# Kernel tuning notes

Measured on AMD Instinct MI355X. Metric: run time of the kernel, lower is better.

## Reference

```python
import jax, jax.numpy as jnp
import numpy as np

K = 20  # hard-coded in LPDNet


def act(v):
    # LeakyReLU with negative_slope=0.0 == ReLU
    return jnp.maximum(v, 0.0)


def conv1d(x, w, b):
    # x: (B,C,N), w: (O,C), b: (O,) -> (B,O,N)  (1x1 Conv1d)
    return jnp.einsum('bcn,oc->bon', x, w) + b[None, :, None]


def conv2d(x, w, b):
    # x: (B,C,N,K), w: (O,C), b: (O,) -> (B,O,N,K)  (1x1 Conv2d)
    return jnp.einsum('bcnk,oc->bonk', x, w) + b[None, :, None, None]


def knn(x, k):
    # x: (B,C,N) -> idx (B,N,k) of nearest neighbors by negative squared L2
    xx = jnp.sum(x * x, axis=1)                       # (B,N)
    inner = jnp.einsum('bcn,bcm->bnm', x, x)          # (B,N,N)
    pairwise = 2.0 * inner - xx[:, :, None] - xx[:, None, :]
    _, idx = jax.lax.top_k(pairwise, k)
    return idx


def graph_feature(x, idx):
    # x: (B,C,N), idx: (B,N,k) -> (B,2C,N,k) as concat(neighbor - center, center)
    xt = jnp.transpose(x, (0, 2, 1))                  # (B,N,C)
    nbr = jax.vmap(lambda f, i: f[i])(xt, idx)        # (B,N,k,C)
    ctr = jnp.broadcast_to(xt[:, :, None, :], nbr.shape)
    feat = jnp.concatenate([nbr - ctr, ctr], axis=-1)  # (B,N,k,2C)
    return jnp.transpose(feat, (0, 3, 1, 2))          # (B,2C,N,k)


def setup_inputs():
    key = jax.random.key(0)
    ks = jax.random.split(key, 13)
    p = lambda k, s: jax.random.normal(k, s, jnp.float32) * 0.02
    return {
        'x': jax.random.normal(ks[0], (8, 1, 4096, 3), jnp.float32),
        'w1': p(ks[1], (64, 3)),    'b1': p(ks[2], (64,)),
        'w2': p(ks[3], (64, 64)),   'b2': p(ks[4], (64,)),
        'wdg1': p(ks[5], (128, 128)), 'bdg1': p(ks[6], (128,)),
        'wdg2': p(ks[7], (128, 128)), 'bdg2': p(ks[8], (128,)),
        'wsn1': p(ks[9], (256, 256)), 'bsn1': p(ks[10], (256,)),
        'w3': p(ks[11], (1024, 512)), 'b3': p(ks[12], (1024,)),
    }


def reference(x, w1, b1, w2, b2, wdg1, bdg1, wdg2, bdg2, wsn1, bsn1, w3, b3):
    xp = jnp.transpose(jnp.squeeze(x, 1), (0, 2, 1))  # (B,3,N)
    xinit = xp
    h = act(conv1d(xp, w1, b1))                       # (B,64,N)
    h = act(conv1d(h, w2, b2))                        # (B,64,N)
    idx1 = knn(h, K)
    g = graph_feature(h, idx1)                        # (B,128,N,K)
    g = act(conv2d(g, wdg1, bdg1))                    # (B,128,N,K)
    x1 = jnp.max(g, axis=-1)                          # (B,128,N)
    g = act(conv2d(g, wdg2, bdg2))                    # (B,128,N,K)
    x2 = jnp.max(g, axis=-1)                          # (B,128,N)
    idx2 = knn(xinit, K)                              # knn on raw 3D coords
    g = graph_feature(x2, idx2)                       # (B,256,N,K)
    g = act(conv2d(g, wsn1, bsn1))                    # (B,256,N,K)
    x3 = jnp.max(g, axis=-1)                          # (B,256,N)
    cat = jnp.concatenate([x1, x2, x3], axis=1)       # (B,512,N)
    out = act(conv1d(cat, w3, b3))                    # (B,1024,N)
    return out[..., None]                             # (B,1024,N,1)
```

## Files before the change

### kernel.cpp

```cpp
#include <hip/hip_runtime.h>
#include <stdint.h>


#define NB 8
#define NP 4096
#define NPTS (NB*NP)

typedef float  floatx4 __attribute__((ext_vector_type(4)));
typedef short  short8  __attribute__((ext_vector_type(8)));

__device__ __forceinline__ unsigned short f2bf(float f) {
  union { float f; uint32_t u; } v; v.f = f;
  uint32_t r = v.u + 0x7fffu + ((v.u >> 16) & 1u);
  return (unsigned short)(r >> 16);
}
__device__ __forceinline__ float bf2f(unsigned short h) {
  union { uint32_t u; float f; } v; v.u = ((uint32_t)h) << 16;
  return v.f;
}

__device__ __forceinline__ floatx4 mfma_bf16(short8 a, short8 b, floatx4 c) {
  return __builtin_amdgcn_mfma_f32_16x16x32_bf16(a, b, c, 0, 0, 0);
}

__global__ void cvt_weights(const float* wdg1, unsigned short* wdg1b,
                            const float* wdg2, unsigned short* wdg2b,
                            const float* wsn1, unsigned short* wsn1b,
                            const float* w3, unsigned short* w3b) {
  int i = blockIdx.x * 256 + threadIdx.x;
  if (i < 16384) {
    int c = i & 127;
    wdg1b[i] = f2bf(wdg1[i] - (c >= 64 ? wdg1[i - 64] : 0.f));
  }
  if (i < 16384) wdg2b[i] = f2bf(wdg2[i]);
  if (i < 65536) {
    int c = i & 255;
    wsn1b[i] = f2bf(wsn1[i] - (c >= 128 ? wsn1[i - 128] : 0.f));
  }
  if (i < 524288) w3b[i] = f2bf(w3[i]);
}

__global__ __launch_bounds__(256) void conv12(
    const float* __restrict__ xin, const float* __restrict__ w1,
    const float* __restrict__ b1, const float* __restrict__ w2,
    const float* __restrict__ b2,
    unsigned short* __restrict__ hb16, unsigned short* __restrict__ hlo16,
    float* __restrict__ hh, float* __restrict__ cc) {
  int wave = threadIdx.x >> 6, lane = threadIdx.x & 63;
  int p = blockIdx.x * 4 + wave;
  __shared__ float s_h1[4][64];
  const float* xp = xin + p * 3;
  float c0 = xp[0], c1 = xp[1], c2 = xp[2];
  float v = b1[lane] + w1[lane*3+0]*c0 + w1[lane*3+1]*c1 + w1[lane*3+2]*c2;
  s_h1[wave][lane] = fmaxf(v, 0.f);
  __syncthreads();
  float acc = b2[lane];
  const float* wr = w2 + lane * 64;
  #pragma unroll
  for (int c = 0; c < 64; c += 4) {
    floatx4 w4 = *(const floatx4*)(wr + c);
    acc += w4[0]*s_h1[wave][c]   + w4[1]*s_h1[wave][c+1]
         + w4[2]*s_h1[wave][c+2] + w4[3]*s_h1[wave][c+3];
  }
  acc = fmaxf(acc, 0.f);
  unsigned short hi = f2bf(acc);
  hb16[p*64 + lane] = hi;
  hlo16[p*64 + lane] = f2bf(acc - bf2f(hi));
  float sq = acc * acc;
  #pragma unroll
  for (int off = 32; off; off >>= 1) sq += __shfl_xor(sq, off, 64);
  if (lane == 0) { hh[p] = sq; cc[p] = c0*c0 + c1*c1 + c2*c2; }
}

__global__ __launch_bounds__(256) void knn64_mfma(
    const unsigned short* __restrict__ Hhi, const unsigned short* __restrict__ Hlo,
    const float* __restrict__ XX, int* __restrict__ idx_out) {
  __shared__ unsigned short mhi[64][72];
  __shared__ unsigned short mlo[64][72];
  __shared__ float dots[64][68];
  __shared__ float xxR[64];
  __shared__ float xxM[64];
  __shared__ float tau[64];
  int b = blockIdx.y;
  int r0 = blockIdx.x * 64;
  int t = threadIdx.x;
  int lane = t & 63, wave = t >> 6;
  int quad = lane >> 4, l15 = lane & 15;
  const unsigned short* Hhib = Hhi + (size_t)b * NP * 64;
  const unsigned short* Hlob = Hlo + (size_t)b * NP * 64;
  short8 ahi[2], alo[2];
  {
    const unsigned short* pr = Hhib + (size_t)(r0 + wave * 16 + l15) * 64 + quad * 8;
    const unsigned short* pl = Hlob + (size_t)(r0 + wave * 16 + l15) * 64 + quad * 8;
    ahi[0] = *(const short8*)pr; ahi[1] = *(const short8*)(pr + 32);
    alo[0] = *(const short8*)pl; alo[1] = *(const short8*)(pl + 32);
  }
  if (t < 64) { xxR[t] = XX[b * NP + r0 + t]; tau[t] = -__builtin_inff(); }

  float lv[20]; int li[20];
  #pragma unroll
  for (int s = 0; s < 20; s++) { lv[s] = -__builtin_inff(); li[s] = 0x7fffffff; }
  float minval = -__builtin_inff(); int minpos = 0;
  int row = t >> 2, sub = t & 3;

  for (int mt = 0; mt < NP / 64; mt++) {
    int m0 = mt * 64;
    {
      int pt = t >> 2, c0 = (t & 3) * 16;
      const unsigned short* sh = Hhib + (size_t)(m0 + pt) * 64 + c0;
      const unsigned short* sl = Hlob + (size_t)(m0 + pt) * 64 + c0;
      *(short8*)&mhi[pt][c0]     = *(const short8*)sh;
      *(short8*)&mhi[pt][c0 + 8] = *(const short8*)(sh + 8);
      *(short8*)&mlo[pt][c0]     = *(const short8*)sl;
      *(short8*)&mlo[pt][c0 + 8] = *(const short8*)(sl + 8);
    }
    if (t < 64) xxM[t] = XX[b * NP + m0 + t];
    __syncthreads();
    #pragma unroll
    for (int nt = 0; nt < 4; nt++) {
      floatx4 acc = (floatx4)0.f;
      #pragma unroll
      for (int ks = 0; ks < 2; ks++) {
        int k0 = ks * 32 + quad * 8;
        short8 bhi = *(short8*)&mhi[nt * 16 + l15][k0];
        short8 blo = *(short8*)&mlo[nt * 16 + l15][k0];
        acc = mfma_bf16(ahi[ks], bhi, acc);
        acc = mfma_bf16(ahi[ks], blo, acc);
        acc = mfma_bf16(alo[ks], bhi, acc);
        acc = mfma_bf16(alo[ks], blo, acc);
      }
      int colg = nt * 16 + l15;
      float xm = xxM[colg];
      #pragma unroll
      for (int r = 0; r < 4; r++) {
        int mr = wave * 16 + quad * 4 + r;
        dots[mr][colg] = 2.f * acc[r] - xxR[mr] - xm;
      }
    }
    __syncthreads();
    float gate = fmaxf(minval, tau[row]);
    floatx4 dv0 = *(floatx4*)&dots[row][sub * 16];
    floatx4 dv1 = *(floatx4*)&dots[row][sub * 16 + 4];
    floatx4 dv2 = *(floatx4*)&dots[row][sub * 16 + 8];
    floatx4 dv3 = *(floatx4*)&dots[row][sub * 16 + 12];
    uint32_t mask = 0;
    #pragma unroll
    for (int j = 0; j < 4; j++) {
      if (dv0[j] > gate) mask |= 1u << j;
      if (dv1[j] > gate) mask |= 1u << (4 + j);
      if (dv2[j] > gate) mask |= 1u << (8 + j);
      if (dv3[j] > gate) mask |= 1u << (12 + j);
    }
    #pragma clang loop unroll(disable)
    for (int round = 0; round < 16; round++) {
      if (!__any(mask != 0)) break;
      if (mask) {
        int i = __builtin_ctz(mask); mask &= mask - 1;
        float v = dots[row][sub * 16 + i];
        if (v > minval) {
          int gi = m0 + sub * 16 + i;
          #pragma unroll
          for (int s = 0; s < 20; s++)
            if (s == minpos) { lv[s] = v; li[s] = gi; }
          minval = __builtin_inff();
          #pragma unroll
          for (int s = 0; s < 20; s++)
            if (lv[s] < minval) { minval = lv[s]; minpos = s; }
        }
      }
    }
    tau[row] = fmaxf(tau[row], minval);
  }
  int base = (b * NP + r0 + row) * 20;
  for (int sel = 0; sel < 20; sel++) {
    float mybv = -__builtin_inff(); int mybi = 0x7fffffff, mybs = 0;
    #pragma unroll
    for (int s = 0; s < 20; s++) {
      bool better = lv[s] > mybv || (lv[s] == mybv && li[s] < mybi);
      if (better) { mybv = lv[s]; mybi = li[s]; mybs = s; }
    }
    float bv = mybv; int bi = mybi;
    float ov = __shfl_xor(bv, 1, 64); int oi = __shfl_xor(bi, 1, 64);
    if (ov > bv || (ov == bv && oi < bi)) { bv = ov; bi = oi; }
    ov = __shfl_xor(bv, 2, 64); oi = __shfl_xor(bi, 2, 64);
    if (ov > bv || (ov == bv && oi < bi)) { bv = ov; bi = oi; }
    if (sub == 0) idx_out[base + sel] = bi;
    if (bi == mybi) {
      #pragma unroll
      for (int s = 0; s < 20; s++)
        if (s == mybs) { lv[s] = -__builtin_inff(); li[s] = 0x7fffffff; }
    }
  }
}

template<int C>
__global__ __launch_bounds__(256) void knn_topk(
    const float* __restrict__ X, const float* __restrict__ XX,
    int* __restrict__ idx_out) {
  __shared__ float rowsT[C][68];
  __shared__ float mT[C][68];
  __shared__ float dots[64][68];
  __shared__ float xxR[64];
  __shared__ float xxM[64];
  __shared__ float tau[64];
  int b = blockIdx.y;
  int r0 = blockIdx.x * 64;
  int t = threadIdx.x;
  const float* Xb = X + (size_t)b * NP * C;
  for (int e = t; e < C * 64; e += 256) {
    int r = e / C, c = e - r * C;
    rowsT[c][r] = Xb[(r0 + r) * C + c];
  }
  if (t < 64) { xxR[t] = XX[b * NP + r0 + t]; tau[t] = -__builtin_inff(); }

  float lv[20]; int li[20];
  #pragma unroll
  for (int s = 0; s < 20; s++) { lv[s] = -__builtin_inff(); li[s] = 0x7fffffff; }
  float minval = -__builtin_inff(); int minpos = 0;

  int tm = t & 15, tr = t >> 4;
  int row = t >> 2, sub = t & 3;

  for (int mt = 0; mt < NP / 64; mt++) {
    int m0 = mt * 64;
    for (int e = t; e < C * 64; e += 256) {
      int r = e / C, c = e - r * C;
      mT[c][r] = Xb[(m0 + r) * C + c];
    }
    if (t < 64) xxM[t] = XX[b * NP + m0 + t];
    __syncthreads();
    float acc[4][4];
    #pragma unroll
    for (int i = 0; i < 4; i++)
      #pragma unroll
      for (int j = 0; j < 4; j++) acc[i][j] = 0.f;
    for (int c = 0; c < C; c++) {
      floatx4 av = *(floatx4*)&rowsT[c][tr * 4];
      floatx4 bv = *(floatx4*)&mT[c][tm * 4];
      #pragma unroll
      for (int i = 0; i < 4; i++)
        #pragma unroll
        for (int j = 0; j < 4; j++) acc[i][j] += av[i] * bv[j];
    }
    #pragma unroll
    for (int i = 0; i < 4; i++) {
      floatx4 sv;
      #pragma unroll
      for (int j = 0; j < 4; j++)
        sv[j] = 2.f * acc[i][j] - xxR[tr*4 + i] - xxM[tm*4 + j];
      *(floatx4*)&dots[tr*4 + i][tm*4] = sv;
    }
    __syncthreads();
    float gate = fmaxf(minval, tau[row]);
    floatx4 dv0 = *(floatx4*)&dots[row][sub * 16];
    floatx4 dv1 = *(floatx4*)&dots[row][sub * 16 + 4];
    floatx4 dv2 = *(floatx4*)&dots[row][sub * 16 + 8];
    floatx4 dv3 = *(floatx4*)&dots[row][sub * 16 + 12];
    uint32_t mask = 0;
    #pragma unroll
    for (int j = 0; j < 4; j++) {
      if (dv0[j] > gate) mask |= 1u << j;
      if (dv1[j] > gate) mask |= 1u << (4 + j);
      if (dv2[j] > gate) mask |= 1u << (8 + j);
      if (dv3[j] > gate) mask |= 1u << (12 + j);
    }
    #pragma clang loop unroll(disable)
    for (int round = 0; round < 16; round++) {
      if (!__any(mask != 0)) break;
      if (mask) {
        int i = __builtin_ctz(mask); mask &= mask - 1;
        float v = dots[row][sub * 16 + i];
        if (v > minval) {
          int gi = m0 + sub * 16 + i;
          #pragma unroll
          for (int s = 0; s < 20; s++)
            if (s == minpos) { lv[s] = v; li[s] = gi; }
          minval = __builtin_inff();
          #pragma unroll
          for (int s = 0; s < 20; s++)
            if (lv[s] < minval) { minval = lv[s]; minpos = s; }
        }
      }
    }
    tau[row] = fmaxf(tau[row], minval);
  }
  int base = (b * NP + r0 + row) * 20;
  for (int sel = 0; sel < 20; sel++) {
    float mybv = -__builtin_inff(); int mybi = 0x7fffffff, mybs = 0;
    #pragma unroll
    for (int s = 0; s < 20; s++) {
      bool better = lv[s] > mybv || (lv[s] == mybv && li[s] < mybi);
      if (better) { mybv = lv[s]; mybi = li[s]; mybs = s; }
    }
    float bv = mybv; int bi = mybi;
    float ov = __shfl_xor(bv, 1, 64); int oi = __shfl_xor(bi, 1, 64);
    if (ov > bv || (ov == bv && oi < bi)) { bv = ov; bi = oi; }
    ov = __shfl_xor(bv, 2, 64); oi = __shfl_xor(bi, 2, 64);
    if (ov > bv || (ov == bv && oi < bi)) { bv = ov; bi = oi; }
    if (sub == 0) idx_out[base + sel] = bi;
    if (bi == mybi) {
      #pragma unroll
      for (int s = 0; s < 20; s++)
        if (s == mybs) { lv[s] = -__builtin_inff(); li[s] = 0x7fffffff; }
    }
  }
}

__global__ __launch_bounds__(256) void dg_stage(
    const unsigned short* __restrict__ hb16, const int* __restrict__ idx1,
    const unsigned short* __restrict__ w1b, const float* __restrict__ bia1,
    const unsigned short* __restrict__ w2b, const float* __restrict__ bia2,
    unsigned short* __restrict__ featb) {
  __shared__ unsigned short s_a[80][136];
  __shared__ unsigned short s_v[80][136];
  __shared__ int s_nbf[80];
  int p0 = blockIdx.x * 4;
  int b = p0 >> 12, n0 = p0 & 4095;
  int t = threadIdx.x;
  int lane = t & 63, wave = t >> 6;
  if (t < 80) s_nbf[t] = idx1[p0 * 20 + t];
  __syncthreads();
  const unsigned short* hbb = hb16 + (size_t)b * NP * 64;
  {
    int cc = (t & 15) * 8;
    int r00 = t >> 4;
    #pragma unroll
    for (int it = 0; it < 5; it++) {
      int row = r00 + it * 16;
      const unsigned short* src = (cc < 64)
        ? hbb + (size_t)s_nbf[row] * 64 + cc
        : hbb + (size_t)(n0 + row / 20) * 64 + (cc - 64);
      *(short8*)&s_a[row][cc] = *(const short8*)src;
    }
  }
  __syncthreads();
  int quad = lane >> 4, mrow = lane & 15;
  int nblock = wave * 32;
  {
    floatx4 acc[5][2];
    #pragma unroll
    for (int mt = 0; mt < 5; mt++) { acc[mt][0] = (floatx4)0.f; acc[mt][1] = (floatx4)0.f; }
    #pragma unroll
    for (int ks = 0; ks < 4; ks++) {
      int k0 = ks * 32 + quad * 8;
      short8 w0 = *(const short8*)(w1b + (nblock + mrow) * 128 + k0);
      short8 w1v = *(const short8*)(w1b + (nblock + 16 + mrow) * 128 + k0);
      #pragma unroll
      for (int mt = 0; mt < 5; mt++) {
        short8 a = *(short8*)&s_a[mt * 16 + mrow][k0];
        acc[mt][0] = mfma_bf16(a, w0, acc[mt][0]);
        acc[mt][1] = mfma_bf16(a, w1v, acc[mt][1]);
      }
    }
    #pragma unroll
    for (int ns = 0; ns < 2; ns++) {
      int o = nblock + ns * 16 + mrow;
      float bz = bia1[o];
      #pragma unroll
      for (int mt = 0; mt < 5; mt++)
        #pragma unroll
        for (int r = 0; r < 4; r++)
          s_v[mt * 16 + quad * 4 + r][o] = f2bf(fmaxf(acc[mt][ns][r] + bz, 0.f));
    }
  }
  __syncthreads();
  #pragma unroll
  for (int it = 0; it < 2; it++) {
    int e = t + it * 256;
    int pt = e >> 7, o = e & 127;
    float mx = 0.f;
    for (int k = 0; k < 20; k++) mx = fmaxf(mx, bf2f(s_v[pt * 20 + k][o]));
    featb[(size_t)(p0 + pt) * 512 + o] = f2bf(mx);
  }
  {
    floatx4 acc[5][2];
    #pragma unroll
    for (int mt = 0; mt < 5; mt++) { acc[mt][0] = (floatx4)0.f; acc[mt][1] = (floatx4)0.f; }
    #pragma unroll
    for (int ks = 0; ks < 4; ks++) {
      int k0 = ks * 32 + quad * 8;
      short8 w0 = *(const short8*)(w2b + (nblock + mrow) * 128 + k0);
      short8 w1v = *(const short8*)(w2b + (nblock + 16 + mrow) * 128 + k0);
      #pragma unroll
      for (int mt = 0; mt < 5; mt++) {
        short8 a = *(short8*)&s_v[mt * 16 + mrow][k0];
        acc[mt][0] = mfma_bf16(a, w0, acc[mt][0]);
        acc[mt][1] = mfma_bf16(a, w1v, acc[mt][1]);
      }
    }
    #pragma unroll
    for (int ns = 0; ns < 2; ns++) {
      int o = nblock + ns * 16 + mrow;
      float bz = bia2[o];
      #pragma unroll
      for (int mt = 0; mt < 5; mt++)
        #pragma unroll
        for (int r = 0; r < 4; r++)
          s_a[mt * 16 + quad * 4 + r][o] = f2bf(fmaxf(acc[mt][ns][r] + bz, 0.f));
    }
  }
  __syncthreads();
  #pragma unroll
  for (int it = 0; it < 2; it++) {
    int e = t + it * 256;
    int pt = e >> 7, o = e & 127;
    float mx = 0.f;
    for (int k = 0; k < 20; k++) mx = fmaxf(mx, bf2f(s_a[pt * 20 + k][o]));
    featb[(size_t)(p0 + pt) * 512 + 128 + o] = f2bf(mx);
  }
}

__global__ __launch_bounds__(256) void sn_stage(
    const int* __restrict__ idx2, const unsigned short* __restrict__ wb,
    const float* __restrict__ bias, unsigned short* __restrict__ featb) {
  __shared__ unsigned short s_a[80][264];
  __shared__ int s_nbf[80];
  int p0 = blockIdx.x * 4;
  int b = p0 >> 12, n0 = p0 & 4095;
  int bb = b << 12;
  int t = threadIdx.x;
  int lane = t & 63, wave = t >> 6;
  if (t < 80) s_nbf[t] = idx2[p0 * 20 + t];
  __syncthreads();
  {
    int cc = (t & 31) * 8;
    int r00 = t >> 5;
    #pragma unroll
    for (int it = 0; it < 10; it++) {
      int row = r00 + it * 8;
      const unsigned short* src = (cc < 128)
        ? featb + (size_t)(bb + s_nbf[row]) * 512 + 128 + cc
        : featb + (size_t)(bb + n0 + row / 20) * 512 + cc;
      *(short8*)&s_a[row][cc] = *(const short8*)src;
    }
  }
  __syncthreads();
  int quad = lane >> 4, mrow = lane & 15;
  int nblock = wave * 64;
  floatx4 acc[5][4];
  #pragma unroll
  for (int mt = 0; mt < 5; mt++)
    #pragma unroll
    for (int ns = 0; ns < 4; ns++) acc[mt][ns] = (floatx4)0.f;
  #pragma unroll
  for (int ks = 0; ks < 8; ks++) {
    int k0 = ks * 32 + quad * 8;
    short8 w[4];
    #pragma unroll
    for (int ns = 0; ns < 4; ns++)
      w[ns] = *(const short8*)(wb + (nblock + ns * 16 + mrow) * 256 + k0);
    #pragma unroll
    for (int mt = 0; mt < 5; mt++) {
      short8 a = *(short8*)&s_a[mt * 16 + mrow][k0];
      #pragma unroll
      for (int ns = 0; ns < 4; ns++)
        acc[mt][ns] = mfma_bf16(a, w[ns], acc[mt][ns]);
    }
  }
  __syncthreads();
  #pragma unroll
  for (int ns = 0; ns < 4; ns++) {
    int o = nblock + ns * 16 + mrow;
    float bz = bias[o];
    #pragma unroll
    for (int mt = 0; mt < 5; mt++)
      #pragma unroll
      for (int r = 0; r < 4; r++)
        s_a[mt * 16 + quad * 4 + r][o] = f2bf(fmaxf(acc[mt][ns][r] + bz, 0.f));
  }
  __syncthreads();
  #pragma unroll
  for (int it = 0; it < 4; it++) {
    int e = t + it * 256;
    int pt = e >> 8, o = e & 255;
    float mx = 0.f;
    for (int k = 0; k < 20; k++) mx = fmaxf(mx, bf2f(s_a[pt * 20 + k][o]));
    featb[(size_t)(p0 + pt) * 512 + 256 + o] = f2bf(mx);
  }
}

__global__ __launch_bounds__(256) void conv3_gemm(
    const unsigned short* __restrict__ w3b, const unsigned short* __restrict__ featb,
    const float* __restrict__ b3, float* __restrict__ out) {
  __shared__ unsigned short s_a[128][40];
  __shared__ unsigned short s_b[128][40];
  int o0 = blockIdx.x * 128, p0 = blockIdx.y * 128;
  int t = threadIdx.x, lane = t & 63, wave = t >> 6;
  int wy = wave >> 1, wx = wave & 1;
  int quad = lane >> 4, l15 = lane & 15;
  floatx4 acc[4][4];
  #pragma unroll
  for (int i = 0; i < 4; i++)
    #pragma unroll
    for (int j = 0; j < 4; j++) acc[i][j] = (floatx4)0.f;
  for (int kc = 0; kc < 16; kc++) {
    __syncthreads();
    for (int e = t; e < 512; e += 256) {
      int r = e >> 2, c8 = (e & 3) * 8;
      *(short8*)&s_a[r][c8] = *(const short8*)(w3b + (size_t)(o0 + r) * 512 + kc * 32 + c8);
    }
    for (int e = t; e < 512; e += 256) {
      int r = e >> 2, c8 = (e & 3) * 8;
      *(short8*)&s_b[r][c8] = *(const short8*)(featb + (size_t)(p0 + r) * 512 + kc * 32 + c8);
    }
    __syncthreads();
    int k0 = quad * 8;
    short8 af[4], bfr[4];
    #pragma unroll
    for (int i = 0; i < 4; i++) af[i] = *(short8*)&s_a[wy * 64 + i * 16 + l15][k0];
    #pragma unroll
    for (int j = 0; j < 4; j++) bfr[j] = *(short8*)&s_b[wx * 64 + j * 16 + l15][k0];
    #pragma unroll
    for (int i = 0; i < 4; i++)
      #pragma unroll
      for (int j = 0; j < 4; j++) acc[i][j] = mfma_bf16(af[i], bfr[j], acc[i][j]);
  }
  #pragma unroll
  for (int i = 0; i < 4; i++)
    #pragma unroll
    for (int j = 0; j < 4; j++) {
      int pl = p0 + wx * 64 + j * 16 + l15;
      int bI = pl >> 12, n = pl & 4095;
      #pragma unroll
      for (int r = 0; r < 4; r++) {
        int o = o0 + wy * 64 + i * 16 + quad * 4 + r;
        out[(size_t)(bI * 1024 + o) * 4096 + n] = fmaxf(acc[i][j][r] + b3[o], 0.f);
      }
    }
}

extern "C" void kernel_launch(void* const* d_in, const int* in_sizes, int n_in,
                              void* d_out, int out_size, void* d_ws, size_t ws_size,
                              hipStream_t stream) {
  const float* x    = (const float*)d_in[0];
  const float* w1   = (const float*)d_in[1];
  const float* b1   = (const float*)d_in[2];
  const float* w2   = (const float*)d_in[3];
  const float* b2   = (const float*)d_in[4];
  const float* wdg1 = (const float*)d_in[5];
  const float* bdg1 = (const float*)d_in[6];
  const float* wdg2 = (const float*)d_in[7];
  const float* bdg2 = (const float*)d_in[8];
  const float* wsn1 = (const float*)d_in[9];
  const float* bsn1 = (const float*)d_in[10];
  const float* w3   = (const float*)d_in[11];
  const float* b3   = (const float*)d_in[12];

  float* ws = (float*)d_ws;
  unsigned short* hlo16 = (unsigned short*)ws;
  float* hh = ws + 2097152;
  float* cc = ws + 2129920;
  int* idx1 = (int*)(ws + 2162688);
  int* idx2 = (int*)(ws + 2818048);
  unsigned short* featb = (unsigned short*)(ws + 3473408);
  unsigned short* wdg1b = (unsigned short*)(ws + 11862016);
  unsigned short* wdg2b = (unsigned short*)(ws + 11870208);
  unsigned short* wsn1b = (unsigned short*)(ws + 11878400);
  unsigned short* w3b   = (unsigned short*)(ws + 11911168);
  unsigned short* hb16  = (unsigned short*)(ws + 12173312);

  cvt_weights<<<2048, 256, 0, stream>>>(wdg1, wdg1b, wdg2, wdg2b,
                                        wsn1, wsn1b, w3, w3b);
  conv12<<<8192, 256, 0, stream>>>(x, w1, b1, w2, b2, hb16, hlo16, hh, cc);
  knn64_mfma<<<dim3(64, 8), 256, 0, stream>>>(hb16, hlo16, hh, idx1);
  knn_topk<3><<<dim3(64, 8), 256, 0, stream>>>(x, cc, idx2);
  dg_stage<<<8192, 256, 0, stream>>>(hb16, idx1, wdg1b, bdg1, wdg2b, bdg2, featb);
  sn_stage<<<8192, 256, 0, stream>>>(idx2, wsn1b, bsn1, featb);
  conv3_gemm<<<dim3(8, 256), 256, 0, stream>>>(w3b, featb, b3, (float*)d_out);
}
```

Measured before the change: 1.077 ms.

## Split KNN candidate scan into two halves and merge partial top-20 lists

Both KNN kernels now run on a grid with a z dimension of 2, each block scanning half of the candidate points and writing a sorted partial top-20 (values and indices) to workspace. A new merge40 kernel merges the two sorted lists per row into the final 20 indices. This doubles the block count from 512 to 1024 so the GPU's compute units are better occupied, at the cost of extra global writes, two extra launches, and reusing the featb workspace region as temporary storage.

```diff
diff --git a/kernel.cpp b/kernel.cpp
--- a/kernel.cpp
+++ b/kernel.cpp
@@ -74,7 +74,8 @@
 
 __global__ __launch_bounds__(256) void knn64_mfma(
     const unsigned short* __restrict__ Hhi, const unsigned short* __restrict__ Hlo,
-    const float* __restrict__ XX, int* __restrict__ idx_out) {
+    const float* __restrict__ XX, float* __restrict__ val_out,
+    int* __restrict__ idxp_out) {
   __shared__ unsigned short mhi[64][72];
   __shared__ unsigned short mlo[64][72];
   __shared__ float dots[64][68];
@@ -83,6 +84,7 @@
   __shared__ float tau[64];
   int b = blockIdx.y;
   int r0 = blockIdx.x * 64;
+  int half = blockIdx.z;
   int t = threadIdx.x;
   int lane = t & 63, wave = t >> 6;
   int quad = lane >> 4, l15 = lane & 15;
@@ -103,7 +105,8 @@
   float minval = -__builtin_inff(); int minpos = 0;
   int row = t >> 2, sub = t & 3;
 
-  for (int mt = 0; mt < NP / 64; mt++) {
+  int mt0 = half * (NP / 128);
+  for (int mt = mt0; mt < mt0 + NP / 128; mt++) {
     int m0 = mt * 64;
     {
       int pt = t >> 2, c0 = (t & 3) * 16;
@@ -171,7 +174,7 @@
     }
     tau[row] = fmaxf(tau[row], minval);
   }
-  int base = (b * NP + r0 + row) * 20;
+  int base = ((b * NP + r0 + row) * 2 + half) * 20;
   for (int sel = 0; sel < 20; sel++) {
     float mybv = -__builtin_inff(); int mybi = 0x7fffffff, mybs = 0;
     #pragma unroll
@@ -184,7 +187,7 @@
     if (ov > bv || (ov == bv && oi < bi)) { bv = ov; bi = oi; }
     ov = __shfl_xor(bv, 2, 64); oi = __shfl_xor(bi, 2, 64);
     if (ov > bv || (ov == bv && oi < bi)) { bv = ov; bi = oi; }
-    if (sub == 0) idx_out[base + sel] = bi;
+    if (sub == 0) { val_out[base + sel] = bv; idxp_out[base + sel] = bi; }
     if (bi == mybi) {
       #pragma unroll
       for (int s = 0; s < 20; s++)
@@ -196,7 +199,7 @@
 template<int C>
 __global__ __launch_bounds__(256) void knn_topk(
     const float* __restrict__ X, const float* __restrict__ XX,
-    int* __restrict__ idx_out) {
+    float* __restrict__ val_out, int* __restrict__ idxp_out) {
   __shared__ float rowsT[C][68];
   __shared__ float mT[C][68];
   __shared__ float dots[64][68];
@@ -205,6 +208,7 @@
   __shared__ float tau[64];
   int b = blockIdx.y;
   int r0 = blockIdx.x * 64;
+  int half = blockIdx.z;
   int t = threadIdx.x;
   const float* Xb = X + (size_t)b * NP * C;
   for (int e = t; e < C * 64; e += 256) {
@@ -221,7 +225,8 @@
   int tm = t & 15, tr = t >> 4;
   int row = t >> 2, sub = t & 3;
 
-  for (int mt = 0; mt < NP / 64; mt++) {
+  int mt0 = half * (NP / 128);
+  for (int mt = mt0; mt < mt0 + NP / 128; mt++) {
     int m0 = mt * 64;
     for (int e = t; e < C * 64; e += 256) {
       int r = e / C, c = e - r * C;
@@ -284,7 +289,7 @@
     }
     tau[row] = fmaxf(tau[row], minval);
   }
-  int base = (b * NP + r0 + row) * 20;
+  int base = ((b * NP + r0 + row) * 2 + half) * 20;
   for (int sel = 0; sel < 20; sel++) {
     float mybv = -__builtin_inff(); int mybi = 0x7fffffff, mybs = 0;
     #pragma unroll
@@ -297,12 +302,30 @@
     if (ov > bv || (ov == bv && oi < bi)) { bv = ov; bi = oi; }
     ov = __shfl_xor(bv, 2, 64); oi = __shfl_xor(bi, 2, 64);
     if (ov > bv || (ov == bv && oi < bi)) { bv = ov; bi = oi; }
-    if (sub == 0) idx_out[base + sel] = bi;
+    if (sub == 0) { val_out[base + sel] = bv; idxp_out[base + sel] = bi; }
     if (bi == mybi) {
       #pragma unroll
       for (int s = 0; s < 20; s++)
         if (s == mybs) { lv[s] = -__builtin_inff(); li[s] = 0x7fffffff; }
     }
+  }
+}
+
+__global__ __launch_bounds__(256) void merge40(
+    const float* __restrict__ val, const int* __restrict__ midx,
+    int* __restrict__ idx_out) {
+  int r = blockIdx.x * 256 + threadIdx.x;
+  const float* vA = val + (size_t)r * 40;
+  const int*   iA = midx + (size_t)r * 40;
+  int a = 0, bp = 20;
+  int base = r * 20;
+  #pragma unroll
+  for (int s = 0; s < 20; s++) {
+    float va = vA[a], vb = vA[bp];
+    int ia = iA[a], ib = iA[bp];
+    bool takeA = (va > vb) || (va == vb && ia < ib);
+    idx_out[base + s] = takeA ? ia : ib;
+    if (takeA) a++; else bp++;
   }
 }
 
@@ -559,11 +582,18 @@
   unsigned short* w3b   = (unsigned short*)(ws + 11911168);
   unsigned short* hb16  = (unsigned short*)(ws + 12173312);
 
+  float* c1val = ws + 3473408;
+  int*   c1idx = (int*)(ws + 4784128);
+  float* c2val = ws + 6094848;
+  int*   c2idx = (int*)(ws + 7405568);
+
   cvt_weights<<<2048, 256, 0, stream>>>(wdg1, wdg1b, wdg2, wdg2b,
                                         wsn1, wsn1b, w3, w3b);
   conv12<<<8192, 256, 0, stream>>>(x, w1, b1, w2, b2, hb16, hlo16, hh, cc);
-  knn64_mfma<<<dim3(64, 8), 256, 0, stream>>>(hb16, hlo16, hh, idx1);
-  knn_topk<3><<<dim3(64, 8), 256, 0, stream>>>(x, cc, idx2);
+  knn64_mfma<<<dim3(64, 8, 2), 256, 0, stream>>>(hb16, hlo16, hh, c1val, c1idx);
+  knn_topk<3><<<dim3(64, 8, 2), 256, 0, stream>>>(x, cc, c2val, c2idx);
+  merge40<<<128, 256, 0, stream>>>(c1val, c1idx, idx1);
+  merge40<<<128, 256, 0, stream>>>(c2val, c2idx, idx2);
   dg_stage<<<8192, 256, 0, stream>>>(hb16, idx1, wdg1b, bdg1, wdg2b, bdg2, featb);
   sn_stage<<<8192, 256, 0, stream>>>(idx2, wsn1b, bsn1, featb);
   conv3_gemm<<<dim3(8, 256), 256, 0, stream>>>(w3b, featb, b3, (float*)d_out);
```

Measured after the change: 1.101 ms. 2.2% more time.

## Widen kNN column tile to 128 and drop row-constant distance terms

Applied to the files above, without the earlier changes.

The MFMA kNN kernel now processes 128 candidate columns per iteration instead of 64, halving the number of loop iterations and barriers and giving each lane 32 candidates to scan. Both kNN kernels replace the score 2*dot - xx_r - xx_m with dot - 0.5*xx_m. The dropped term is constant per row and the rest is a positive rescale, so the ranking is unchanged. The wider tile increases shared memory and register use (8 float4 per thread), which may reduce occupancy, and the rescaled score can change tie behaviour slightly due to rounding.

```diff
diff --git a/kernel.cpp b/kernel.cpp
--- a/kernel.cpp
+++ b/kernel.cpp
@@ -75,11 +75,10 @@
 __global__ __launch_bounds__(256) void knn64_mfma(
     const unsigned short* __restrict__ Hhi, const unsigned short* __restrict__ Hlo,
     const float* __restrict__ XX, int* __restrict__ idx_out) {
-  __shared__ unsigned short mhi[64][72];
-  __shared__ unsigned short mlo[64][72];
-  __shared__ float dots[64][68];
-  __shared__ float xxR[64];
-  __shared__ float xxM[64];
+  __shared__ unsigned short mhi[128][72];
+  __shared__ unsigned short mlo[128][72];
+  __shared__ float dots[64][132];
+  __shared__ float xxMh[128];
   __shared__ float tau[64];
   int b = blockIdx.y;
   int r0 = blockIdx.x * 64;
@@ -95,7 +94,7 @@
     ahi[0] = *(const short8*)pr; ahi[1] = *(const short8*)(pr + 32);
     alo[0] = *(const short8*)pl; alo[1] = *(const short8*)(pl + 32);
   }
-  if (t < 64) { xxR[t] = XX[b * NP + r0 + t]; tau[t] = -__builtin_inff(); }
+  if (t < 64) tau[t] = -__builtin_inff();
 
   float lv[20]; int li[20];
   #pragma unroll
@@ -103,21 +102,26 @@
   float minval = -__builtin_inff(); int minpos = 0;
   int row = t >> 2, sub = t & 3;
 
-  for (int mt = 0; mt < NP / 64; mt++) {
-    int m0 = mt * 64;
+  for (int mt = 0; mt < NP / 128; mt++) {
+    int m0 = mt * 128;
     {
-      int pt = t >> 2, c0 = (t & 3) * 16;
-      const unsigned short* sh = Hhib + (size_t)(m0 + pt) * 64 + c0;
-      const unsigned short* sl = Hlob + (size_t)(m0 + pt) * 64 + c0;
-      *(short8*)&mhi[pt][c0]     = *(const short8*)sh;
-      *(short8*)&mhi[pt][c0 + 8] = *(const short8*)(sh + 8);
-      *(short8*)&mlo[pt][c0]     = *(const short8*)sl;
-      *(short8*)&mlo[pt][c0 + 8] = *(const short8*)(sl + 8);
-    }
-    if (t < 64) xxM[t] = XX[b * NP + m0 + t];
+      int hf = t & 1, r = (t >> 1) & 127;
+      int c0 = hf * 32;
+      const unsigned short* sh = Hhib + (size_t)(m0 + r) * 64 + c0;
+      const unsigned short* sl = Hlob + (size_t)(m0 + r) * 64 + c0;
+      *(short8*)&mhi[r][c0]      = *(const short8*)sh;
+      *(short8*)&mhi[r][c0 + 8]  = *(const short8*)(sh + 8);
+      *(short8*)&mhi[r][c0 + 16] = *(const short8*)(sh + 16);
+      *(short8*)&mhi[r][c0 + 24] = *(const short8*)(sh + 24);
+      *(short8*)&mlo[r][c0]      = *(const short8*)sl;
+      *(short8*)&mlo[r][c0 + 8]  = *(const short8*)(sl + 8);
+      *(short8*)&mlo[r][c0 + 16] = *(const short8*)(sl + 16);
+      *(short8*)&mlo[r][c0 + 24] = *(const short8*)(sl + 24);
+    }
+    if (t < 128) xxMh[t] = 0.5f * XX[b * NP + m0 + t];
     __syncthreads();
     #pragma unroll
-    for (int nt = 0; nt < 4; nt++) {
+    for (int nt = 0; nt < 8; nt++) {
       floatx4 acc = (floatx4)0.f;
       #pragma unroll
       for (int ks = 0; ks < 2; ks++) {
@@ -130,12 +134,121 @@
         acc = mfma_bf16(alo[ks], blo, acc);
       }
       int colg = nt * 16 + l15;
-      float xm = xxM[colg];
+      float xm = xxMh[colg];
       #pragma unroll
       for (int r = 0; r < 4; r++) {
         int mr = wave * 16 + quad * 4 + r;
-        dots[mr][colg] = 2.f * acc[r] - xxR[mr] - xm;
-      }
+        dots[mr][colg] = acc[r] - xm;
+      }
+    }
+    __syncthreads();
+    float gate = fmaxf(minval, tau[row]);
+    floatx4 dv[8];
+    #pragma unroll
+    for (int q = 0; q < 8; q++) dv[q] = *(floatx4*)&dots[row][sub * 32 + q * 4];
+    uint32_t mask = 0;
+    #pragma unroll
+    for (int q = 0; q < 8; q++)
+      #pragma unroll
+      for (int j = 0; j < 4; j++)
+        if (dv[q][j] > gate) mask |= 1u << (q * 4 + j);
+    #pragma clang loop unroll(disable)
+    for (int round = 0; round < 32; round++) {
+      if (!__any(mask != 0)) break;
+      if (mask) {
+        int i = __builtin_ctz(mask); mask &= mask - 1;
+        float v = dots[row][sub * 32 + i];
+        if (v > minval) {
+          int gi = m0 + sub * 32 + i;
+          #pragma unroll
+          for (int s = 0; s < 20; s++)
+            if (s == minpos) { lv[s] = v; li[s] = gi; }
+          minval = __builtin_inff();
+          #pragma unroll
+          for (int s = 0; s < 20; s++)
+            if (lv[s] < minval) { minval = lv[s]; minpos = s; }
+        }
+      }
+    }
+    tau[row] = fmaxf(tau[row], minval);
+  }
+  int base = (b * NP + r0 + row) * 20;
+  for (int sel = 0; sel < 20; sel++) {
+    float mybv = -__builtin_inff(); int mybi = 0x7fffffff, mybs = 0;
+    #pragma unroll
+    for (int s = 0; s < 20; s++) {
+      bool better = lv[s] > mybv || (lv[s] == mybv && li[s] < mybi);
+      if (better) { mybv = lv[s]; mybi = li[s]; mybs = s; }
+    }
+    float bv = mybv; int bi = mybi;
+    float ov = __shfl_xor(bv, 1, 64); int oi = __shfl_xor(bi, 1, 64);
+    if (ov > bv || (ov == bv && oi < bi)) { bv = ov; bi = oi; }
+    ov = __shfl_xor(bv, 2, 64); oi = __shfl_xor(bi, 2, 64);
+    if (ov > bv || (ov == bv && oi < bi)) { bv = ov; bi = oi; }
+    if (sub == 0) idx_out[base + sel] = bi;
+    if (bi == mybi) {
+      #pragma unroll
+      for (int s = 0; s < 20; s++)
+        if (s == mybs) { lv[s] = -__builtin_inff(); li[s] = 0x7fffffff; }
+    }
+  }
+}
+
+template<int C>
+__global__ __launch_bounds__(256) void knn_topk(
+    const float* __restrict__ X, const float* __restrict__ XX,
+    int* __restrict__ idx_out) {
+  __shared__ float rowsT[C][68];
+  __shared__ float mT[C][68];
+  __shared__ float dots[64][68];
+  __shared__ float xxMh[64];
+  __shared__ float tau[64];
+  int b = blockIdx.y;
+  int r0 = blockIdx.x * 64;
+  int t = threadIdx.x;
+  const float* Xb = X + (size_t)b * NP * C;
+  for (int e = t; e < C * 64; e += 256) {
+    int r = e / C, c = e - r * C;
+    rowsT[c][r] = Xb[(r0 + r) * C + c];
+  }
+  if (t < 64) tau[t] = -__builtin_inff();
+
+  float lv[20]; int li[20];
+  #pragma unroll
+  for (int s = 0; s < 20; s++) { lv[s] = -__builtin_inff(); li[s] = 0x7fffffff; }
+  float minval = -__builtin_inff(); int minpos = 0;
+
+  int tm = t & 15, tr = t >> 4;
+  int row = t >> 2, sub = t & 3;
+
+  for (int mt = 0; mt < NP / 64; mt++) {
+    int m0 = mt * 64;
+    for (int e = t; e < C * 64; e += 256) {
+      int r = e / C, c = e - r * C;
+      mT[c][r] = Xb[(m0 + r) * C + c];
+    }
+    if (t < 64) xxMh[t] = 0.5f * XX[b * NP + m0 + t];
+    __syncthreads();
+    float acc[4][4];
+    #pragma unroll
+    for (int i = 0; i < 4; i++)
+      #pragma unroll
+      for (int j = 0; j < 4; j++) acc[i][j] = 0.f;
+    for (int c = 0; c < C; c++) {
+      floatx4 av = *(floatx4*)&rowsT[c][tr * 4];
+      floatx4 bv = *(floatx4*)&mT[c][tm * 4];
+      #pragma unroll
+      for (int i = 0; i < 4; i++)
+        #pragma unroll
+        for (int j = 0; j < 4; j++) acc[i][j] += av[i] * bv[j];
+    }
+    #pragma unroll
+    for (int i = 0; i < 4; i++) {
+      floatx4 sv;
+      #pragma unroll
+      for (int j = 0; j < 4; j++)
+        sv[j] = acc[i][j] - xxMh[tm*4 + j];
+      *(floatx4*)&dots[tr*4 + i][tm*4] = sv;
     }
     __syncthreads();
     float gate = fmaxf(minval, tau[row]);
@@ -193,119 +306,6 @@
   }
 }
 
-template<int C>
-__global__ __launch_bounds__(256) void knn_topk(
-    const float* __restrict__ X, const float* __restrict__ XX,
-    int* __restrict__ idx_out) {
-  __shared__ float rowsT[C][68];
-  __shared__ float mT[C][68];
-  __shared__ float dots[64][68];
-  __shared__ float xxR[64];
-  __shared__ float xxM[64];
-  __shared__ float tau[64];
-  int b = blockIdx.y;
-  int r0 = blockIdx.x * 64;
-  int t = threadIdx.x;
-  const float* Xb = X + (size_t)b * NP * C;
-  for (int e = t; e < C * 64; e += 256) {
-    int r = e / C, c = e - r * C;
-    rowsT[c][r] = Xb[(r0 + r) * C + c];
-  }
-  if (t < 64) { xxR[t] = XX[b * NP + r0 + t]; tau[t] = -__builtin_inff(); }
-
-  float lv[20]; int li[20];
-  #pragma unroll
-  for (int s = 0; s < 20; s++) { lv[s] = -__builtin_inff(); li[s] = 0x7fffffff; }
-  float minval = -__builtin_inff(); int minpos = 0;
-
-  int tm = t & 15, tr = t >> 4;
-  int row = t >> 2, sub = t & 3;
-
-  for (int mt = 0; mt < NP / 64; mt++) {
-    int m0 = mt * 64;
-    for (int e = t; e < C * 64; e += 256) {
-      int r = e / C, c = e - r * C;
-      mT[c][r] = Xb[(m0 + r) * C + c];
-    }
-    if (t < 64) xxM[t] = XX[b * NP + m0 + t];
-    __syncthreads();
-    float acc[4][4];
-    #pragma unroll
-    for (int i = 0; i < 4; i++)
-      #pragma unroll
-      for (int j = 0; j < 4; j++) acc[i][j] = 0.f;
-    for (int c = 0; c < C; c++) {
-      floatx4 av = *(floatx4*)&rowsT[c][tr * 4];
-      floatx4 bv = *(floatx4*)&mT[c][tm * 4];
-      #pragma unroll
-      for (int i = 0; i < 4; i++)
-        #pragma unroll
-        for (int j = 0; j < 4; j++) acc[i][j] += av[i] * bv[j];
-    }
-    #pragma unroll
-    for (int i = 0; i < 4; i++) {
-      floatx4 sv;
-      #pragma unroll
-      for (int j = 0; j < 4; j++)
-        sv[j] = 2.f * acc[i][j] - xxR[tr*4 + i] - xxM[tm*4 + j];
-      *(floatx4*)&dots[tr*4 + i][tm*4] = sv;
-    }
-    __syncthreads();
-    float gate = fmaxf(minval, tau[row]);
-    floatx4 dv0 = *(floatx4*)&dots[row][sub * 16];
-    floatx4 dv1 = *(floatx4*)&dots[row][sub * 16 + 4];
-    floatx4 dv2 = *(floatx4*)&dots[row][sub * 16 + 8];
-    floatx4 dv3 = *(floatx4*)&dots[row][sub * 16 + 12];
-    uint32_t mask = 0;
-    #pragma unroll
-    for (int j = 0; j < 4; j++) {
-      if (dv0[j] > gate) mask |= 1u << j;
-      if (dv1[j] > gate) mask |= 1u << (4 + j);
-      if (dv2[j] > gate) mask |= 1u << (8 + j);
-      if (dv3[j] > gate) mask |= 1u << (12 + j);
-    }
-    #pragma clang loop unroll(disable)
-    for (int round = 0; round < 16; round++) {
-      if (!__any(mask != 0)) break;
-      if (mask) {
-        int i = __builtin_ctz(mask); mask &= mask - 1;
-        float v = dots[row][sub * 16 + i];
-        if (v > minval) {
-          int gi = m0 + sub * 16 + i;
-          #pragma unroll
-          for (int s = 0; s < 20; s++)
-            if (s == minpos) { lv[s] = v; li[s] = gi; }
-          minval = __builtin_inff();
-          #pragma unroll
-          for (int s = 0; s < 20; s++)
-            if (lv[s] < minval) { minval = lv[s]; minpos = s; }
-        }
-      }
-    }
-    tau[row] = fmaxf(tau[row], minval);
-  }
-  int base = (b * NP + r0 + row) * 20;
-  for (int sel = 0; sel < 20; sel++) {
-    float mybv = -__builtin_inff(); int mybi = 0x7fffffff, mybs = 0;
-    #pragma unroll
-    for (int s = 0; s < 20; s++) {
-      bool better = lv[s] > mybv || (lv[s] == mybv && li[s] < mybi);
-      if (better) { mybv = lv[s]; mybi = li[s]; mybs = s; }
-    }
-    float bv = mybv; int bi = mybi;
-    float ov = __shfl_xor(bv, 1, 64); int oi = __shfl_xor(bi, 1, 64);
-    if (ov > bv || (ov == bv && oi < bi)) { bv = ov; bi = oi; }
-    ov = __shfl_xor(bv, 2, 64); oi = __shfl_xor(bi, 2, 64);
-    if (ov > bv || (ov == bv && oi < bi)) { bv = ov; bi = oi; }
-    if (sub == 0) idx_out[base + sel] = bi;
-    if (bi == mybi) {
-      #pragma unroll
-      for (int s = 0; s < 20; s++)
-        if (s == mybs) { lv[s] = -__builtin_inff(); li[s] = 0x7fffffff; }
-    }
-  }
-}
-
 __global__ __launch_bounds__(256) void dg_stage(
     const unsigned short* __restrict__ hb16, const int* __restrict__ idx1,
     const unsigned short* __restrict__ w1b, const float* __restrict__ bia1,
```

Measured after the change: 1.033 ms. -4.1%, faster.
